# Kernel tuning notes

Measured on AMD Instinct MI355X. Metric: run time of the kernel, lower is better.

## Reference

```python
import jax, jax.numpy as jnp
import numpy as np

B, T, E = 4, 2048, 768
HN, HS = 12, 64          # head_num, head_size = E // HN
L = 6                    # n_layer
FF = 4 * E
O = 1                    # output_dim
EPS = 1e-5


def setup_inputs() -> dict:
    key = jax.random.key(0)
    ks = iter(jax.random.split(key, 40))
    r = lambda shape, s=0.02: jax.random.normal(next(ks), shape, jnp.float32) * s
    inp = {
        'idx': jax.random.normal(next(ks), (B, T, E), jnp.float32),
        'hidden': jnp.zeros((1, B, E), jnp.float32),
        # per-layer, per-head q/k/v linears
        'wq': r((L, HN, E, HS)), 'bq': jnp.zeros((L, HN, HS), jnp.float32),
        'wk': r((L, HN, E, HS)), 'bk': jnp.zeros((L, HN, HS), jnp.float32),
        'wv': r((L, HN, E, HS)), 'bv': jnp.zeros((L, HN, HS), jnp.float32),
        'wproj': r((L, E, E)), 'bproj': jnp.zeros((L, E), jnp.float32),
        'ln1_g': jnp.ones((L, E), jnp.float32), 'ln1_b': jnp.zeros((L, E), jnp.float32),
        'ln2_g': jnp.ones((L, E), jnp.float32), 'ln2_b': jnp.zeros((L, E), jnp.float32),
        'w1': r((L, E, FF)), 'b1': jnp.zeros((L, FF), jnp.float32),
        'w2': r((L, FF, E)), 'b2': jnp.zeros((L, E), jnp.float32),
        'lnf_g': jnp.ones((E,), jnp.float32), 'lnf_b': jnp.zeros((E,), jnp.float32),
        'fw1': r((E, FF)), 'fb1': jnp.zeros((FF,), jnp.float32),
        'fw2': r((FF, E)), 'fb2': jnp.zeros((E,), jnp.float32),
        'hw': r((E, O)), 'hb': jnp.zeros((O,), jnp.float32),
    }
    return inp


def _layernorm(x, g, b):
    m = jnp.mean(x, axis=-1, keepdims=True)
    v = jnp.var(x, axis=-1, keepdims=True)
    return (x - m) * jax.lax.rsqrt(v + EPS) * g + b


def _forward(idx, wq, bq, wk, bk, wv, bv, wproj, bproj,
             ln1_g, ln1_b, ln2_g, ln2_b, w1, b1, w2, b2,
             lnf_g, lnf_b, fw1, fb1, fw2, fb2, hw, hb):
    x = idx
    Bn, Tn, En = x.shape
    causal = jnp.tril(jnp.ones((Tn, Tn), bool))  # [T,T]
    scale = 1.0 / jnp.sqrt(jnp.asarray(En, x.dtype))  # NOTE: divides by sqrt(n_embed), as in source
    for l in range(wq.shape[0]):
        h = _layernorm(x, ln1_g[l], ln1_b[l])
        q = jnp.einsum('bte,hes->bhts', h, wq[l]) + bq[l][None, :, None, :]
        k = jnp.einsum('bte,hes->bhts', h, wk[l]) + bk[l][None, :, None, :]
        v = jnp.einsum('bte,hes->bhts', h, wv[l]) + bv[l][None, :, None, :]
        scores = jnp.einsum('bhts,bhus->bhtu', q, k) * scale
        scores = jnp.where(causal, scores, -jnp.inf)
        att = jax.nn.softmax(scores, axis=-1)
        o = jnp.einsum('bhtu,bhus->bhts', att, v)          # [B,HN,T,HS]
        o = o.transpose(0, 2, 1, 3).reshape(Bn, Tn, En)     # concat heads
        x = x + o @ wproj[l] + bproj[l]
        h = _layernorm(x, ln2_g[l], ln2_b[l])
        ff = jax.nn.gelu(h @ w1[l] + b1[l], approximate=False) @ w2[l] + b2[l]
        x = x + ff
    x = _layernorm(x, lnf_g, lnf_b)
    x = jax.nn.gelu(x @ fw1 + fb1, approximate=False) @ fw2 + fb2
    logits = x @ hw + hb            # [B,T,O]
    logits = logits[-1]             # [T,O]  (source: logits[-1,:,:])
    return jnp.squeeze(logits, axis=-1)  # [T]


def reference(idx, hidden, wq, bq, wk, bk, wv, bv, wproj, bproj,
              ln1_g, ln1_b, ln2_g, ln2_b, w1, b1, w2, b2,
              lnf_g, lnf_b, fw1, fb1, fw2, fb2, hw, hb):
    # hidden is accepted but unused by the original module.
    del hidden
    return _forward(idx, wq, bq, wk, bk, wv, bv, wproj, bproj,
                    ln1_g, ln1_b, ln2_g, ln2_b, w1, b1, w2, b2,
                    lnf_g, lnf_b, fw1, fb1, fw2, fb2, hw, hb)
```

## Files before the change

### kernel.cpp

```cpp
#include <hip/hip_runtime.h>
#include <math.h>

#define TT 2048
#define EE 768
#define HNN 12
#define HSS 64
#define NLAYER 6
#define FFD 3072
#define QKVN 2304

constexpr float LN_EPS = 1e-5f;
constexpr float ATT_SCALE = 0.03608439182435161f;
constexpr float ATT_SCALE_L2E = 0.03608439182435161f * 1.4426950408889634f;

typedef __attribute__((ext_vector_type(8))) short bf16x8;
typedef __attribute__((ext_vector_type(4))) float f32x4;

__device__ __forceinline__ ushort f2bf(float f) {
    union { float f; uint u; } c; c.f = f;
    const uint u = c.u;
    return (ushort)((u + 0x7fffu + ((u >> 16) & 1u)) >> 16);
}

__device__ __forceinline__ void gload16(const void* g, void* l) {
    __builtin_amdgcn_global_load_lds((const __attribute__((address_space(1))) void*)g,
                                     (__attribute__((address_space(3))) void*)l, 16, 0, 0);
}

__global__ __launch_bounds__(256) void copy4_kernel(float4* __restrict__ dst,
                                                    const float4* __restrict__ src, int n4) {
    int i = blockIdx.x * 256 + threadIdx.x;
    if (i < n4) dst[i] = src[i];
}

__global__ __launch_bounds__(256) void ln_kernel(const float* __restrict__ in,
                                                 const float* __restrict__ g,
                                                 const float* __restrict__ b,
                                                 ushort* __restrict__ out) {
    __shared__ float red[8];
    const int t = blockIdx.x;
    const int tid = threadIdx.x;
    const float* row = in + (size_t)t * EE;
    float v0 = row[tid], v1 = row[tid + 256], v2 = row[tid + 512];
    float s = v0 + v1 + v2;
#pragma unroll
    for (int m = 1; m < 64; m <<= 1) s += __shfl_xor(s, m, 64);
    if ((tid & 63) == 0) red[tid >> 6] = s;
    __syncthreads();
    const float mean = (red[0] + red[1] + red[2] + red[3]) * (1.0f / EE);
    const float d0 = v0 - mean, d1 = v1 - mean, d2 = v2 - mean;
    float qq = d0 * d0 + d1 * d1 + d2 * d2;
#pragma unroll
    for (int m = 1; m < 64; m <<= 1) qq += __shfl_xor(qq, m, 64);
    __syncthreads();
    if ((tid & 63) == 0) red[tid >> 6] = qq;
    __syncthreads();
    const float var = (red[0] + red[1] + red[2] + red[3]) * (1.0f / EE);
    const float rstd = rsqrtf(var + LN_EPS);
    ushort* orow = out + (size_t)t * EE;
    orow[tid]       = f2bf(d0 * rstd * g[tid]       + b[tid]);
    orow[tid + 256] = f2bf(d1 * rstd * g[tid + 256] + b[tid + 256]);
    orow[tid + 512] = f2bf(d2 * rstd * g[tid + 512] + b[tid + 512]);
}

__device__ __forceinline__ void transpose64(const float* __restrict__ src, int sld,
                                            ushort* __restrict__ dst, int dld,
                                            int k0, int n0, int tid) {
    __shared__ float t[64][68];
#pragma unroll
    for (int p = 0; p < 4; p++) {
        const int kr = p * 16 + (tid >> 4);
        *(float4*)&t[kr][(tid & 15) * 4] =
            *(const float4*)&src[(size_t)(k0 + kr) * sld + n0 + (tid & 15) * 4];
    }
    __syncthreads();
#pragma unroll
    for (int q = 0; q < 2; q++) {
        const int nl = q * 32 + (tid >> 3);
        const int kc = (tid & 7) * 8;
        ushort v[8];
#pragma unroll
        for (int j = 0; j < 8; j++) v[j] = f2bf(t[kc + j][nl]);
        uint4 o;
        o.x = (uint)v[0] | ((uint)v[1] << 16);
        o.y = (uint)v[2] | ((uint)v[3] << 16);
        o.z = (uint)v[4] | ((uint)v[5] << 16);
        o.w = (uint)v[6] | ((uint)v[7] << 16);
        *(uint4*)&dst[(size_t)(n0 + nl) * dld + k0 + kc] = o;
    }
}

__global__ __launch_bounds__(256) void pack_t_kernel(const float* __restrict__ src, int sld,
                                                     ushort* __restrict__ dst, int dld) {
    transpose64(src, sld, dst, dld, blockIdx.x * 64, blockIdx.y * 64, threadIdx.x);
}

__global__ __launch_bounds__(256) void pack_qkv_kernel(const float* __restrict__ wq,
                                                       const float* __restrict__ wk,
                                                       const float* __restrict__ wv,
                                                       ushort* __restrict__ dst) {
    const int z = blockIdx.z;
    const int which = z / HNN, hd = z % HNN;
    const float* src = (which == 0 ? wq : which == 1 ? wk : wv) + (size_t)hd * EE * HSS;
    ushort* d = dst + (size_t)(which * EE + hd * HSS) * EE;
    transpose64(src, HSS, d, EE, blockIdx.x * 64, 0, threadIdx.x);
}

__global__ __launch_bounds__(256) void vtrans_kernel(const ushort* __restrict__ qkv,
                                                     ushort* __restrict__ vT) {
    const int t = blockIdx.x * 256 + threadIdx.x;
    const int d = t & 63;
    const int rest = t >> 6;
    const int tb = rest & 255;
    const int hd = rest >> 8;
    const ushort* src = qkv + 1536 + hd * 64 + d;
    ushort v[8];
#pragma unroll
    for (int j = 0; j < 8; j++) v[j] = src[(size_t)(tb * 8 + j) * QKVN];
    uint4 o;
    o.x = (uint)v[0] | ((uint)v[1] << 16);
    o.y = (uint)v[2] | ((uint)v[3] << 16);
    o.z = (uint)v[4] | ((uint)v[5] << 16);
    o.w = (uint)v[6] | ((uint)v[7] << 16);
    *(uint4*)&vT[((size_t)hd * 64 + d) * TT + tb * 8] = o;
}

template <int EPI>
__global__ __launch_bounds__(256) void gemm_bf16(const ushort* __restrict__ A,
                                                 const ushort* __restrict__ Bt,
                                                 const float* __restrict__ b0,
                                                 const float* __restrict__ b1,
                                                 const float* __restrict__ b2,
                                                 float* __restrict__ outF,
                                                 ushort* __restrict__ outB,
                                                 int N, int K,
                                                 int nby, int KS, int Kslice) {
    __shared__ ushort Al[2][128 * 32];
    __shared__ ushort Bl[2][128 * 32];
    const int tid = threadIdx.x;
    const int wave = tid >> 6, lane = tid & 63;
    const int wm = wave >> 1, wn = wave & 1;
    const int l15 = lane & 15, q4 = lane >> 4;

    const int nwg = gridDim.x;
    const int wgid = ((int)blockIdx.x & 7) * (nwg >> 3) + ((int)blockIdx.x >> 3);
    const int mb = wgid % nby;
    const int t2 = wgid / nby;
    const int ks = t2 % KS;
    const int nb = t2 / KS;
    const int m0 = mb * 128, n0 = nb * 128;
    const int kbase = ks * Kslice;

    const int srow = lane >> 2;
    const int scb = (lane & 3) ^ ((lane >> 3) & 3);
    const ushort* Ag0 = A + (size_t)(m0 + wave * 16 + srow) * K + kbase + scb * 8;
    const ushort* Ag1 = Ag0 + (size_t)64 * K;
    const ushort* Bg0 = Bt + (size_t)(n0 + wave * 16 + srow) * K + kbase + scb * 8;
    const ushort* Bg1 = Bg0 + (size_t)64 * K;

    auto stage = [&](int buf, int kk) {
        const int off = kk * 32;
        gload16(Ag0 + off, &Al[buf][(wave * 16) * 32]);
        gload16(Ag1 + off, &Al[buf][(64 + wave * 16) * 32]);
        gload16(Bg0 + off, &Bl[buf][(wave * 16) * 32]);
        gload16(Bg1 + off, &Bl[buf][(64 + wave * 16) * 32]);
    };

    f32x4 acc[4][4];
#pragma unroll
    for (int i = 0; i < 4; i++)
#pragma unroll
        for (int j = 0; j < 4; j++) acc[i][j] = (f32x4){0.f, 0.f, 0.f, 0.f};

    stage(0, 0);
    __syncthreads();

    const int niter = Kslice >> 5;
    const int cq = (q4 ^ ((l15 >> 1) & 3)) * 8;

    for (int i = 0; i < niter; i++) {
        const int buf = i & 1;
        if (i + 1 < niter) stage(buf ^ 1, i + 1);
        bf16x8 af[4], bfr[4];
#pragma unroll
        for (int ii = 0; ii < 4; ii++)
            af[ii] = *(const bf16x8*)&Al[buf][(wm * 64 + ii * 16 + l15) * 32 + cq];
#pragma unroll
        for (int j = 0; j < 4; j++)
            bfr[j] = *(const bf16x8*)&Bl[buf][(wn * 64 + j * 16 + l15) * 32 + cq];
#pragma unroll
        for (int ii = 0; ii < 4; ii++)
#pragma unroll
            for (int j = 0; j < 4; j++)
                acc[ii][j] = __builtin_amdgcn_mfma_f32_16x16x32_bf16(af[ii], bfr[j], acc[ii][j], 0, 0, 0);
        __syncthreads();
    }

#pragma unroll
    for (int i = 0; i < 4; i++) {
        const int row = m0 + wm * 64 + i * 16 + q4 * 4;
#pragma unroll
        for (int j = 0; j < 4; j++) {
            const int col = n0 + wn * 64 + j * 16 + l15;
            float bias;
            if constexpr (EPI == 0)
                bias = (col < 768) ? b0[col] : (col < 1536 ? b1[col - 768] : b2[col - 1536]);
            else
                bias = (EPI == 1 && ks != 0) ? 0.f : b0[col];
#pragma unroll
            for (int r = 0; r < 4; r++) {
                const float v = acc[i][j][r] + bias;
                const size_t idx = (size_t)(row + r) * N + col;
                if constexpr (EPI == 0) {
                    outB[idx] = f2bf(v);
                } else if constexpr (EPI == 1) {
                    atomicAdd(&outF[idx], v);
                } else if constexpr (EPI == 2) {
                    outB[idx] = f2bf(0.5f * v * (1.0f + erff(v * 0.70710678118654752f)));
                } else {
                    outF[idx] = v;
                }
            }
        }
    }
}

__global__ __launch_bounds__(256, 2) void attn_mfma(const ushort* __restrict__ qkv,
                                                    const ushort* __restrict__ vT,
                                                    ushort* __restrict__ o_bf) {
    __shared__ __align__(16) uint Ps[4][16 * 36];

    const int tid = threadIdx.x;
    const int wave = tid >> 6, lane = tid & 63;
    const int l15 = lane & 15, q4 = lane >> 4;

    const int x = (int)blockIdx.x & 7, r = (int)blockIdx.x >> 3;
    const int rho = wave * 48 + r;
    int head, qi;
    if (rho < 128) { head = x;           qi = 127 - rho; }
    else           { head = 8 + (x >> 1); qi = 2 * (191 - rho) + (x & 1); }
    const int nkt = (qi >> 2) + 1;
    const int qrow_g = qi * 16 + l15;

    const ushort* qp = qkv + (size_t)qrow_g * QKVN + head * 64;
    const bf16x8 qa0 = *(const bf16x8*)&qp[q4 * 8];
    const bf16x8 qa1 = *(const bf16x8*)&qp[32 + q4 * 8];

    const ushort* kbase = qkv + 768 + head * 64 + (size_t)l15 * QKVN + q4 * 8;
    const ushort* vbase = vT + ((size_t)head * 64 + l15) * TT + q4 * 8;

    float m_i = -1e30f, l_i = 0.f;
    f32x4 oacc[4];
#pragma unroll
    for (int n = 0; n < 4; n++) oacc[n] = (f32x4){0.f, 0.f, 0.f, 0.f};

    bf16x8 kA[8], kB[8], vC[8];
#pragma unroll
    for (int n = 0; n < 4; n++)
#pragma unroll
        for (int kb = 0; kb < 2; kb++)
            kA[n * 2 + kb] = *(const bf16x8*)(kbase + (size_t)(n * 16) * QKVN + kb * 32);

    uint* psrow = &Ps[wave][l15 * 36];

    auto body = [&](bf16x8* kc, bf16x8* kn, int kt) {
        const ushort* vp = vbase + kt * 64;
#pragma unroll
        for (int n = 0; n < 4; n++)
#pragma unroll
            for (int kb = 0; kb < 2; kb++)
                vC[n * 2 + kb] = *(const bf16x8*)(vp + (size_t)(n * 16) * TT + kb * 32);
        if (kt + 1 < nkt) {
            const ushort* kp = kbase + (size_t)(kt + 1) * 64 * QKVN;
#pragma unroll
            for (int n = 0; n < 4; n++)
#pragma unroll
                for (int kb = 0; kb < 2; kb++)
                    kn[n * 2 + kb] = *(const bf16x8*)(kp + (size_t)(n * 16) * QKVN + kb * 32);
        }
        f32x4 s[4];
#pragma unroll
        for (int n = 0; n < 4; n++) {
            f32x4 a = (f32x4){0.f, 0.f, 0.f, 0.f};
            a = __builtin_amdgcn_mfma_f32_16x16x32_bf16(kc[n * 2], qa0, a, 0, 0, 0);
            a = __builtin_amdgcn_mfma_f32_16x16x32_bf16(kc[n * 2 + 1], qa1, a, 0, 0, 0);
            s[n] = a;
        }
        float pe[16];
        const bool diag = (kt == nkt - 1);
#pragma unroll
        for (int n = 0; n < 4; n++) {
            const int k0 = kt * 64 + n * 16 + q4 * 4;
#pragma unroll
            for (int rr = 0; rr < 4; rr++) {
                float xv = s[n][rr] * ATT_SCALE_L2E;
                if (diag && (k0 + rr) > qrow_g) xv = -1e30f;
                pe[n * 4 + rr] = xv;
            }
        }
        float t8[8];
#pragma unroll
        for (int i = 0; i < 8; i++) t8[i] = fmaxf(pe[i], pe[i + 8]);
        float mx = fmaxf(fmaxf(fmaxf(t8[0], t8[4]), fmaxf(t8[1], t8[5])),
                         fmaxf(fmaxf(t8[2], t8[6]), fmaxf(t8[3], t8[7])));
        mx = fmaxf(mx, __shfl_xor(mx, 16, 64));
        mx = fmaxf(mx, __shfl_xor(mx, 32, 64));
        const float nm = fmaxf(m_i, mx);
        const float al = exp2f(m_i - nm);
#pragma unroll
        for (int i = 0; i < 16; i++) pe[i] = exp2f(pe[i] - nm);
        float s8[8];
#pragma unroll
        for (int i = 0; i < 8; i++) s8[i] = pe[i] + pe[i + 8];
        float rs = ((s8[0] + s8[4]) + (s8[1] + s8[5])) + ((s8[2] + s8[6]) + (s8[3] + s8[7]));
        rs += __shfl_xor(rs, 16, 64);
        rs += __shfl_xor(rs, 32, 64);
        l_i = l_i * al + rs;
        m_i = nm;
        float alr[4];
#pragma unroll
        for (int rr = 0; rr < 4; rr++) alr[rr] = __shfl(al, q4 * 4 + rr, 64);
#pragma unroll
        for (int n = 0; n < 4; n++) {
            oacc[n][0] *= alr[0];
            oacc[n][1] *= alr[1];
            oacc[n][2] *= alr[2];
            oacc[n][3] *= alr[3];
        }
#pragma unroll
        for (int n = 0; n < 4; n++) {
            uint2 d2;
            d2.x = (uint)f2bf(pe[n * 4 + 0]) | ((uint)f2bf(pe[n * 4 + 1]) << 16);
            d2.y = (uint)f2bf(pe[n * 4 + 2]) | ((uint)f2bf(pe[n * 4 + 3]) << 16);
            *(uint2*)&psrow[(8 * n + 2 * q4 + 4 * l15) & 31] = d2;
        }
        const bf16x8 pa0 = *(const bf16x8*)&psrow[(4 * q4 + 4 * l15) & 31];
        const bf16x8 pa1 = *(const bf16x8*)&psrow[(16 + 4 * q4 + 4 * l15) & 31];
#pragma unroll
        for (int n = 0; n < 4; n++) {
            oacc[n] = __builtin_amdgcn_mfma_f32_16x16x32_bf16(pa0, vC[n * 2], oacc[n], 0, 0, 0);
            oacc[n] = __builtin_amdgcn_mfma_f32_16x16x32_bf16(pa1, vC[n * 2 + 1], oacc[n], 0, 0, 0);
        }
    };

    int kt = 0;
    for (;;) {
        body(kA, kB, kt);
        if (++kt >= nkt) break;
        body(kB, kA, kt);
        if (++kt >= nkt) break;
    }

    float lrec[4];
#pragma unroll
    for (int rr = 0; rr < 4; rr++) lrec[rr] = 1.0f / __shfl(l_i, q4 * 4 + rr, 64);
#pragma unroll
    for (int n = 0; n < 4; n++)
#pragma unroll
        for (int rr = 0; rr < 4; rr++)
            o_bf[(size_t)(qi * 16 + q4 * 4 + rr) * EE + head * 64 + n * 16 + l15] =
                f2bf(oacc[n][rr] * lrec[rr]);
}

__global__ __launch_bounds__(256) void head_kernel(const float* __restrict__ x,
                                                   const float* __restrict__ hw,
                                                   const float* __restrict__ hb,
                                                   float* __restrict__ out) {
    __shared__ float red[8];
    const int t = blockIdx.x, tid = threadIdx.x;
    const float* row = x + (size_t)t * EE;
    float s = row[tid] * hw[tid] + row[tid + 256] * hw[tid + 256] + row[tid + 512] * hw[tid + 512];
#pragma unroll
    for (int m = 1; m < 64; m <<= 1) s += __shfl_xor(s, m, 64);
    if ((tid & 63) == 0) red[tid >> 6] = s;
    __syncthreads();
    if (tid == 0) out[t] = red[0] + red[1] + red[2] + red[3] + hb[0];
}

extern "C" void kernel_launch(void* const* d_in, const int* in_sizes, int n_in,
                              void* d_out, int out_size, void* d_ws, size_t ws_size,
                              hipStream_t stream) {
    const float* idx   = (const float*)d_in[0];
    const float* wq    = (const float*)d_in[2];
    const float* bq    = (const float*)d_in[3];
    const float* wk    = (const float*)d_in[4];
    const float* bk    = (const float*)d_in[5];
    const float* wv    = (const float*)d_in[6];
    const float* bv    = (const float*)d_in[7];
    const float* wproj = (const float*)d_in[8];
    const float* bproj = (const float*)d_in[9];
    const float* ln1g  = (const float*)d_in[10];
    const float* ln1b  = (const float*)d_in[11];
    const float* ln2g  = (const float*)d_in[12];
    const float* ln2b  = (const float*)d_in[13];
    const float* w1    = (const float*)d_in[14];
    const float* b1    = (const float*)d_in[15];
    const float* w2    = (const float*)d_in[16];
    const float* b2    = (const float*)d_in[17];
    const float* lnfg  = (const float*)d_in[18];
    const float* lnfb  = (const float*)d_in[19];
    const float* fw1   = (const float*)d_in[20];
    const float* fb1   = (const float*)d_in[21];
    const float* fw2   = (const float*)d_in[22];
    const float* fb2   = (const float*)d_in[23];
    const float* hw    = (const float*)d_in[24];
    const float* hb    = (const float*)d_in[25];
    float* out = (float*)d_out;

    char* p = (char*)d_ws;
    auto alloc = [&](size_t bytes) { void* r = (void*)p; p += (bytes + 255) & ~(size_t)255; return r; };
    float*  x     = (float*)alloc((size_t)TT * EE * 4);
    ushort* h_bf  = (ushort*)alloc((size_t)TT * EE * 2);
    ushort* qkvb  = (ushort*)alloc((size_t)TT * QKVN * 2);
    ushort* o_bf  = (ushort*)alloc((size_t)TT * EE * 2);
    ushort* ffb   = (ushort*)alloc((size_t)TT * FFD * 2);
    ushort* Wqkv  = (ushort*)alloc((size_t)QKVN * EE * 2);
    ushort* Wproj = (ushort*)alloc((size_t)EE * EE * 2);
    ushort* W1t   = (ushort*)alloc((size_t)FFD * EE * 2);
    ushort* W2t   = (ushort*)alloc((size_t)EE * FFD * 2);
    ushort* vTb   = (ushort*)alloc((size_t)HNN * HSS * TT * 2);

    copy4_kernel<<<dim3((TT * EE / 4 + 255) / 256), dim3(256), 0, stream>>>(
        (float4*)x, (const float4*)(idx + (size_t)3 * TT * EE), TT * EE / 4);

    for (int l = 0; l < NLAYER; l++) {
        const size_t lw = (size_t)l;
        pack_qkv_kernel<<<dim3(12, 1, 36), dim3(256), 0, stream>>>(
            wq + lw * HNN * EE * HSS, wk + lw * HNN * EE * HSS, wv + lw * HNN * EE * HSS, Wqkv);
        pack_t_kernel<<<dim3(12, 12), dim3(256), 0, stream>>>(wproj + lw * EE * EE, EE, Wproj, EE);
        pack_t_kernel<<<dim3(12, 48), dim3(256), 0, stream>>>(w1 + lw * EE * FFD, FFD, W1t, EE);
        pack_t_kernel<<<dim3(48, 12), dim3(256), 0, stream>>>(w2 + lw * FFD * EE, EE, W2t, FFD);

        ln_kernel<<<dim3(TT), dim3(256), 0, stream>>>(x, ln1g + lw * EE, ln1b + lw * EE, h_bf);
        gemm_bf16<0><<<dim3(288), dim3(256), 0, stream>>>(
            h_bf, Wqkv, bq + lw * EE, bk + lw * EE, bv + lw * EE, nullptr, qkvb,
            QKVN, EE, 16, 1, EE);
        vtrans_kernel<<<dim3(768), dim3(256), 0, stream>>>(qkvb, vTb);
        attn_mfma<<<dim3(384), dim3(256), 0, stream>>>(qkvb, vTb, o_bf);
        gemm_bf16<1><<<dim3(384), dim3(256), 0, stream>>>(
            o_bf, Wproj, bproj + lw * EE, nullptr, nullptr, x, nullptr,
            EE, EE, 16, 4, 192);
        ln_kernel<<<dim3(TT), dim3(256), 0, stream>>>(x, ln2g + lw * EE, ln2b + lw * EE, h_bf);
        gemm_bf16<2><<<dim3(384), dim3(256), 0, stream>>>(
            h_bf, W1t, b1 + lw * FFD, nullptr, nullptr, nullptr, ffb,
            FFD, EE, 16, 1, EE);
        gemm_bf16<1><<<dim3(384), dim3(256), 0, stream>>>(
            ffb, W2t, b2 + lw * EE, nullptr, nullptr, x, nullptr,
            EE, FFD, 16, 4, 768);
    }

    ln_kernel<<<dim3(TT), dim3(256), 0, stream>>>(x, lnfg, lnfb, h_bf);
    pack_t_kernel<<<dim3(12, 48), dim3(256), 0, stream>>>(fw1, FFD, W1t, EE);
    pack_t_kernel<<<dim3(48, 12), dim3(256), 0, stream>>>(fw2, EE, W2t, FFD);
    gemm_bf16<2><<<dim3(384), dim3(256), 0, stream>>>(
        h_bf, W1t, fb1, nullptr, nullptr, nullptr, ffb, FFD, EE, 16, 1, EE);
    gemm_bf16<3><<<dim3(96), dim3(256), 0, stream>>>(
        ffb, W2t, fb2, nullptr, nullptr, x, nullptr, EE, FFD, 16, 1, FFD);
    head_kernel<<<dim3(TT), dim3(256), 0, stream>>>(x, hw, hb, out);
}
```

Before: 1.620 ms.

## Split long causal attention rows across KV chunks with combine kernel

Attention work is now split into fixed 12-tile KV chunks. Query tiles beyond the first 48 are divided into 2 or 3 partial chunks whose unnormalized outputs and m/l statistics go to a scratch buffer, aliased on the FFN buffer. A new combine kernel merges the partials in flash-decoding style. This evens out per-wave work across the causal triangle and raises occupancy hints, at the cost of an extra launch and extra fp32 traffic through global memory.

```diff
diff --git a/kernel.cpp b/kernel.cpp
--- a/kernel.cpp
+++ b/kernel.cpp
@@ -225,21 +225,27 @@
     }
 }
 
-__global__ __launch_bounds__(256, 2) void attn_mfma(const ushort* __restrict__ qkv,
+__global__ __launch_bounds__(256, 4) void attn_mfma(const ushort* __restrict__ qkv,
                                                     const ushort* __restrict__ vT,
-                                                    ushort* __restrict__ o_bf) {
+                                                    ushort* __restrict__ o_bf,
+                                                    float* __restrict__ pbuf) {
     __shared__ __align__(16) uint Ps[4][16 * 36];
 
     const int tid = threadIdx.x;
     const int wave = tid >> 6, lane = tid & 63;
     const int l15 = lane & 15, q4 = lane >> 4;
 
-    const int x = (int)blockIdx.x & 7, r = (int)blockIdx.x >> 3;
-    const int rho = wave * 48 + r;
-    int head, qi;
-    if (rho < 128) { head = x;           qi = 127 - rho; }
-    else           { head = 8 + (x >> 1); qi = 2 * (191 - rho) + (x & 1); }
+    const int chunk = (int)blockIdx.x * 4 + wave;
+    const int head = chunk / 240;
+    const int t = chunk - head * 240;
+    int qi, c;
+    if (t < 48) { qi = t; c = 0; }
+    else if (t < 144) { const int u = t - 48; qi = 48 + (u >> 1); c = u & 1; }
+    else { const int u = t - 144; const int q3 = u / 3; qi = 96 + q3; c = u - q3 * 3; }
     const int nkt = (qi >> 2) + 1;
+    const int kt_begin = c * 12;
+    const int kt_end = min(kt_begin + 12, nkt);
+    const bool direct = (qi < 48);
     const int qrow_g = qi * 16 + l15;
 
     const ushort* qp = qkv + (size_t)qrow_g * QKVN + head * 64;
@@ -255,11 +261,14 @@
     for (int n = 0; n < 4; n++) oacc[n] = (f32x4){0.f, 0.f, 0.f, 0.f};
 
     bf16x8 kA[8], kB[8], vC[8];
-#pragma unroll
-    for (int n = 0; n < 4; n++)
-#pragma unroll
-        for (int kb = 0; kb < 2; kb++)
-            kA[n * 2 + kb] = *(const bf16x8*)(kbase + (size_t)(n * 16) * QKVN + kb * 32);
+    {
+        const ushort* kp = kbase + (size_t)kt_begin * 64 * QKVN;
+#pragma unroll
+        for (int n = 0; n < 4; n++)
+#pragma unroll
+            for (int kb = 0; kb < 2; kb++)
+                kA[n * 2 + kb] = *(const bf16x8*)(kp + (size_t)(n * 16) * QKVN + kb * 32);
+    }
 
     uint* psrow = &Ps[wave][l15 * 36];
 
@@ -270,7 +279,7 @@
 #pragma unroll
             for (int kb = 0; kb < 2; kb++)
                 vC[n * 2 + kb] = *(const bf16x8*)(vp + (size_t)(n * 16) * TT + kb * 32);
-        if (kt + 1 < nkt) {
+        if (kt + 1 < kt_end) {
             const ushort* kp = kbase + (size_t)(kt + 1) * 64 * QKVN;
 #pragma unroll
             for (int n = 0; n < 4; n++)
@@ -343,23 +352,64 @@
         }
     };
 
-    int kt = 0;
+    int kt = kt_begin;
     for (;;) {
         body(kA, kB, kt);
-        if (++kt >= nkt) break;
+        if (++kt >= kt_end) break;
         body(kB, kA, kt);
-        if (++kt >= nkt) break;
-    }
-
-    float lrec[4];
-#pragma unroll
-    for (int rr = 0; rr < 4; rr++) lrec[rr] = 1.0f / __shfl(l_i, q4 * 4 + rr, 64);
-#pragma unroll
-    for (int n = 0; n < 4; n++)
-#pragma unroll
-        for (int rr = 0; rr < 4; rr++)
-            o_bf[(size_t)(qi * 16 + q4 * 4 + rr) * EE + head * 64 + n * 16 + l15] =
-                f2bf(oacc[n][rr] * lrec[rr]);
+        if (++kt >= kt_end) break;
+    }
+
+    if (direct) {
+        float lrec[4];
+#pragma unroll
+        for (int rr = 0; rr < 4; rr++) lrec[rr] = 1.0f / __shfl(l_i, q4 * 4 + rr, 64);
+#pragma unroll
+        for (int n = 0; n < 4; n++)
+#pragma unroll
+            for (int rr = 0; rr < 4; rr++)
+                o_bf[(size_t)(qi * 16 + q4 * 4 + rr) * EE + head * 64 + n * 16 + l15] =
+                    f2bf(oacc[n][rr] * lrec[rr]);
+    } else {
+        float* pb = pbuf + (size_t)((head * 80 + (qi - 48)) * 3 + c) * 1056;
+#pragma unroll
+        for (int n = 0; n < 4; n++)
+#pragma unroll
+            for (int rr = 0; rr < 4; rr++)
+                pb[(q4 * 4 + rr) * 64 + n * 16 + l15] = oacc[n][rr];
+        if (q4 == 0) {
+            pb[1024 + l15] = m_i;
+            pb[1040 + l15] = l_i;
+        }
+    }
+}
+
+__global__ __launch_bounds__(256) void attn_combine(const float* __restrict__ pbuf,
+                                                    ushort* __restrict__ o_bf) {
+    const int wave = threadIdx.x >> 6, lane = threadIdx.x & 63;
+    const int task = (int)blockIdx.x * 4 + wave;
+    const int head = task / 80;
+    const int u = task - head * 80;
+    const int qi = 48 + u;
+    const int nc = (qi < 96) ? 2 : 3;
+    const float* pb = pbuf + (size_t)((head * 80 + u) * 3) * 1056;
+
+    for (int r = 0; r < 16; r++) {
+        float m0 = pb[1024 + r];
+        float m1 = pb[1056 + 1024 + r];
+        float m2 = (nc == 3) ? pb[2112 + 1024 + r] : -1e30f;
+        const float M = fmaxf(fmaxf(m0, m1), m2);
+        const float w0 = exp2f(m0 - M);
+        const float w1 = exp2f(m1 - M);
+        const float w2 = (nc == 3) ? exp2f(m2 - M) : 0.f;
+        float L = w0 * pb[1040 + r] + w1 * pb[1056 + 1040 + r];
+        float v = w0 * pb[r * 64 + lane] + w1 * pb[1056 + r * 64 + lane];
+        if (nc == 3) {
+            L += w2 * pb[2112 + 1040 + r];
+            v += w2 * pb[2112 + r * 64 + lane];
+        }
+        o_bf[(size_t)(qi * 16 + r) * EE + head * 64 + lane] = f2bf(v / L);
+    }
 }
 
 __global__ __launch_bounds__(256) void head_kernel(const float* __restrict__ x,
@@ -419,6 +469,7 @@
     ushort* W1t   = (ushort*)alloc((size_t)FFD * EE * 2);
     ushort* W2t   = (ushort*)alloc((size_t)EE * FFD * 2);
     ushort* vTb   = (ushort*)alloc((size_t)HNN * HSS * TT * 2);
+    float* pbuf = (float*)ffb;
 
     copy4_kernel<<<dim3((TT * EE / 4 + 255) / 256), dim3(256), 0, stream>>>(
         (float4*)x, (const float4*)(idx + (size_t)3 * TT * EE), TT * EE / 4);
@@ -436,7 +487,8 @@
             h_bf, Wqkv, bq + lw * EE, bk + lw * EE, bv + lw * EE, nullptr, qkvb,
             QKVN, EE, 16, 1, EE);
         vtrans_kernel<<<dim3(768), dim3(256), 0, stream>>>(qkvb, vTb);
-        attn_mfma<<<dim3(384), dim3(256), 0, stream>>>(qkvb, vTb, o_bf);
+        attn_mfma<<<dim3(720), dim3(256), 0, stream>>>(qkvb, vTb, o_bf, pbuf);
+        attn_combine<<<dim3(240), dim3(256), 0, stream>>>(pbuf, o_bf);
         gemm_bf16<1><<<dim3(384), dim3(256), 0, stream>>>(
             o_bf, Wproj, bproj + lw * EE, nullptr, nullptr, x, nullptr,
             EE, EE, 16, 4, 192);
```

New measurement: 1.851 ms. +14.3%, slower.

## Split attention KV range across waves with shared-memory softmax merge

Applied to the files above, without the earlier changes.

Each block now handles one 16-row query tile, and its four waves each process a contiguous quarter of the causal KV tiles (split-K flash attention). Partial outputs, maxima and sums are combined through shared memory with a log-sum-exp merge, and the grid grows from 384 to 1536 blocks. The launch bound is raised to 4 blocks per SM. This is meant to cut the per-wave serial KV loop length and improve load balance and latency hiding. In exchange it adds LDS traffic, a block barrier, and idle waves on short rows where there are fewer than four KV tiles.

```diff
diff --git a/kernel.cpp b/kernel.cpp
--- a/kernel.cpp
+++ b/kernel.cpp
@@ -225,21 +225,26 @@
     }
 }
 
-__global__ __launch_bounds__(256, 2) void attn_mfma(const ushort* __restrict__ qkv,
+__global__ __launch_bounds__(256, 4) void attn_mfma(const ushort* __restrict__ qkv,
                                                     const ushort* __restrict__ vT,
                                                     ushort* __restrict__ o_bf) {
-    __shared__ __align__(16) uint Ps[4][16 * 36];
+    __shared__ __align__(16) uint  Ps[4][16 * 36];
+    __shared__ __align__(16) float Po[4][16 * 64];
+    __shared__ float Pm[4][16];
+    __shared__ float Pl[4][16];
 
     const int tid = threadIdx.x;
     const int wave = tid >> 6, lane = tid & 63;
     const int l15 = lane & 15, q4 = lane >> 4;
 
     const int x = (int)blockIdx.x & 7, r = (int)blockIdx.x >> 3;
-    const int rho = wave * 48 + r;
     int head, qi;
-    if (rho < 128) { head = x;           qi = 127 - rho; }
-    else           { head = 8 + (x >> 1); qi = 2 * (191 - rho) + (x & 1); }
+    if (r < 128) { head = x;            qi = 127 - r; }
+    else         { head = 8 + (x >> 1); qi = 2 * (191 - r) + (x & 1); }
     const int nkt = (qi >> 2) + 1;
+    const int per = (nkt + 3) >> 2;
+    const int kt0 = wave * per;
+    const int kt1 = min(kt0 + per, nkt);
     const int qrow_g = qi * 16 + l15;
 
     const ushort* qp = qkv + (size_t)qrow_g * QKVN + head * 64;
@@ -254,112 +259,140 @@
 #pragma unroll
     for (int n = 0; n < 4; n++) oacc[n] = (f32x4){0.f, 0.f, 0.f, 0.f};
 
-    bf16x8 kA[8], kB[8], vC[8];
+    uint* psrow = &Ps[wave][l15 * 36];
+
+    if (kt0 < kt1) {
+        bf16x8 kA[8], kB[8], vC[8];
+        {
+            const ushort* kp = kbase + (size_t)kt0 * 64 * QKVN;
+#pragma unroll
+            for (int n = 0; n < 4; n++)
+#pragma unroll
+                for (int kb = 0; kb < 2; kb++)
+                    kA[n * 2 + kb] = *(const bf16x8*)(kp + (size_t)(n * 16) * QKVN + kb * 32);
+        }
+
+        auto body = [&](bf16x8* kc, bf16x8* kn, int kt) {
+            const ushort* vp = vbase + kt * 64;
+#pragma unroll
+            for (int n = 0; n < 4; n++)
+#pragma unroll
+                for (int kb = 0; kb < 2; kb++)
+                    vC[n * 2 + kb] = *(const bf16x8*)(vp + (size_t)(n * 16) * TT + kb * 32);
+            if (kt + 1 < kt1) {
+                const ushort* kp = kbase + (size_t)(kt + 1) * 64 * QKVN;
+#pragma unroll
+                for (int n = 0; n < 4; n++)
+#pragma unroll
+                    for (int kb = 0; kb < 2; kb++)
+                        kn[n * 2 + kb] = *(const bf16x8*)(kp + (size_t)(n * 16) * QKVN + kb * 32);
+            }
+            f32x4 s[4];
+#pragma unroll
+            for (int n = 0; n < 4; n++) {
+                f32x4 a = (f32x4){0.f, 0.f, 0.f, 0.f};
+                a = __builtin_amdgcn_mfma_f32_16x16x32_bf16(kc[n * 2], qa0, a, 0, 0, 0);
+                a = __builtin_amdgcn_mfma_f32_16x16x32_bf16(kc[n * 2 + 1], qa1, a, 0, 0, 0);
+                s[n] = a;
+            }
+            float pe[16];
+            const bool diag = (kt == nkt - 1);
+#pragma unroll
+            for (int n = 0; n < 4; n++) {
+                const int k0 = kt * 64 + n * 16 + q4 * 4;
+#pragma unroll
+                for (int rr = 0; rr < 4; rr++) {
+                    float xv = s[n][rr] * ATT_SCALE_L2E;
+                    if (diag && (k0 + rr) > qrow_g) xv = -1e30f;
+                    pe[n * 4 + rr] = xv;
+                }
+            }
+            float t8[8];
+#pragma unroll
+            for (int i = 0; i < 8; i++) t8[i] = fmaxf(pe[i], pe[i + 8]);
+            float mx = fmaxf(fmaxf(fmaxf(t8[0], t8[4]), fmaxf(t8[1], t8[5])),
+                             fmaxf(fmaxf(t8[2], t8[6]), fmaxf(t8[3], t8[7])));
+            mx = fmaxf(mx, __shfl_xor(mx, 16, 64));
+            mx = fmaxf(mx, __shfl_xor(mx, 32, 64));
+            const float nm = fmaxf(m_i, mx);
+            const float al = exp2f(m_i - nm);
+#pragma unroll
+            for (int i = 0; i < 16; i++) pe[i] = exp2f(pe[i] - nm);
+            float s8[8];
+#pragma unroll
+            for (int i = 0; i < 8; i++) s8[i] = pe[i] + pe[i + 8];
+            float rs = ((s8[0] + s8[4]) + (s8[1] + s8[5])) + ((s8[2] + s8[6]) + (s8[3] + s8[7]));
+            rs += __shfl_xor(rs, 16, 64);
+            rs += __shfl_xor(rs, 32, 64);
+            l_i = l_i * al + rs;
+            m_i = nm;
+            float alr[4];
+#pragma unroll
+            for (int rr = 0; rr < 4; rr++) alr[rr] = __shfl(al, q4 * 4 + rr, 64);
+#pragma unroll
+            for (int n = 0; n < 4; n++) {
+                oacc[n][0] *= alr[0];
+                oacc[n][1] *= alr[1];
+                oacc[n][2] *= alr[2];
+                oacc[n][3] *= alr[3];
+            }
+#pragma unroll
+            for (int n = 0; n < 4; n++) {
+                uint2 d2;
+                d2.x = (uint)f2bf(pe[n * 4 + 0]) | ((uint)f2bf(pe[n * 4 + 1]) << 16);
+                d2.y = (uint)f2bf(pe[n * 4 + 2]) | ((uint)f2bf(pe[n * 4 + 3]) << 16);
+                *(uint2*)&psrow[(8 * n + 2 * q4 + 4 * l15) & 31] = d2;
+            }
+            const bf16x8 pa0 = *(const bf16x8*)&psrow[(4 * q4 + 4 * l15) & 31];
+            const bf16x8 pa1 = *(const bf16x8*)&psrow[(16 + 4 * q4 + 4 * l15) & 31];
+#pragma unroll
+            for (int n = 0; n < 4; n++) {
+                oacc[n] = __builtin_amdgcn_mfma_f32_16x16x32_bf16(pa0, vC[n * 2], oacc[n], 0, 0, 0);
+                oacc[n] = __builtin_amdgcn_mfma_f32_16x16x32_bf16(pa1, vC[n * 2 + 1], oacc[n], 0, 0, 0);
+            }
+        };
+
+        int kt = kt0;
+        for (;;) {
+            body(kA, kB, kt);
+            if (++kt >= kt1) break;
+            body(kB, kA, kt);
+            if (++kt >= kt1) break;
+        }
+    }
+
 #pragma unroll
     for (int n = 0; n < 4; n++)
 #pragma unroll
-        for (int kb = 0; kb < 2; kb++)
-            kA[n * 2 + kb] = *(const bf16x8*)(kbase + (size_t)(n * 16) * QKVN + kb * 32);
-
-    uint* psrow = &Ps[wave][l15 * 36];
-
-    auto body = [&](bf16x8* kc, bf16x8* kn, int kt) {
-        const ushort* vp = vbase + kt * 64;
-#pragma unroll
-        for (int n = 0; n < 4; n++)
-#pragma unroll
-            for (int kb = 0; kb < 2; kb++)
-                vC[n * 2 + kb] = *(const bf16x8*)(vp + (size_t)(n * 16) * TT + kb * 32);
-        if (kt + 1 < nkt) {
-            const ushort* kp = kbase + (size_t)(kt + 1) * 64 * QKVN;
-#pragma unroll
-            for (int n = 0; n < 4; n++)
-#pragma unroll
-                for (int kb = 0; kb < 2; kb++)
-                    kn[n * 2 + kb] = *(const bf16x8*)(kp + (size_t)(n * 16) * QKVN + kb * 32);
-        }
-        f32x4 s[4];
-#pragma unroll
-        for (int n = 0; n < 4; n++) {
-            f32x4 a = (f32x4){0.f, 0.f, 0.f, 0.f};
-            a = __builtin_amdgcn_mfma_f32_16x16x32_bf16(kc[n * 2], qa0, a, 0, 0, 0);
-            a = __builtin_amdgcn_mfma_f32_16x16x32_bf16(kc[n * 2 + 1], qa1, a, 0, 0, 0);
-            s[n] = a;
-        }
-        float pe[16];
-        const bool diag = (kt == nkt - 1);
-#pragma unroll
-        for (int n = 0; n < 4; n++) {
-            const int k0 = kt * 64 + n * 16 + q4 * 4;
-#pragma unroll
-            for (int rr = 0; rr < 4; rr++) {
-                float xv = s[n][rr] * ATT_SCALE_L2E;
-                if (diag && (k0 + rr) > qrow_g) xv = -1e30f;
-                pe[n * 4 + rr] = xv;
-            }
-        }
-        float t8[8];
-#pragma unroll
-        for (int i = 0; i < 8; i++) t8[i] = fmaxf(pe[i], pe[i + 8]);
-        float mx = fmaxf(fmaxf(fmaxf(t8[0], t8[4]), fmaxf(t8[1], t8[5])),
-                         fmaxf(fmaxf(t8[2], t8[6]), fmaxf(t8[3], t8[7])));
-        mx = fmaxf(mx, __shfl_xor(mx, 16, 64));
-        mx = fmaxf(mx, __shfl_xor(mx, 32, 64));
-        const float nm = fmaxf(m_i, mx);
-        const float al = exp2f(m_i - nm);
-#pragma unroll
-        for (int i = 0; i < 16; i++) pe[i] = exp2f(pe[i] - nm);
-        float s8[8];
-#pragma unroll
-        for (int i = 0; i < 8; i++) s8[i] = pe[i] + pe[i + 8];
-        float rs = ((s8[0] + s8[4]) + (s8[1] + s8[5])) + ((s8[2] + s8[6]) + (s8[3] + s8[7]));
-        rs += __shfl_xor(rs, 16, 64);
-        rs += __shfl_xor(rs, 32, 64);
-        l_i = l_i * al + rs;
-        m_i = nm;
-        float alr[4];
-#pragma unroll
-        for (int rr = 0; rr < 4; rr++) alr[rr] = __shfl(al, q4 * 4 + rr, 64);
-#pragma unroll
-        for (int n = 0; n < 4; n++) {
-            oacc[n][0] *= alr[0];
-            oacc[n][1] *= alr[1];
-            oacc[n][2] *= alr[2];
-            oacc[n][3] *= alr[3];
-        }
-#pragma unroll
-        for (int n = 0; n < 4; n++) {
-            uint2 d2;
-            d2.x = (uint)f2bf(pe[n * 4 + 0]) | ((uint)f2bf(pe[n * 4 + 1]) << 16);
-            d2.y = (uint)f2bf(pe[n * 4 + 2]) | ((uint)f2bf(pe[n * 4 + 3]) << 16);
-            *(uint2*)&psrow[(8 * n + 2 * q4 + 4 * l15) & 31] = d2;
-        }
-        const bf16x8 pa0 = *(const bf16x8*)&psrow[(4 * q4 + 4 * l15) & 31];
-        const bf16x8 pa1 = *(const bf16x8*)&psrow[(16 + 4 * q4 + 4 * l15) & 31];
-#pragma unroll
-        for (int n = 0; n < 4; n++) {
-            oacc[n] = __builtin_amdgcn_mfma_f32_16x16x32_bf16(pa0, vC[n * 2], oacc[n], 0, 0, 0);
-            oacc[n] = __builtin_amdgcn_mfma_f32_16x16x32_bf16(pa1, vC[n * 2 + 1], oacc[n], 0, 0, 0);
-        }
-    };
-
-    int kt = 0;
-    for (;;) {
-        body(kA, kB, kt);
-        if (++kt >= nkt) break;
-        body(kB, kA, kt);
-        if (++kt >= nkt) break;
-    }
-
-    float lrec[4];
-#pragma unroll
-    for (int rr = 0; rr < 4; rr++) lrec[rr] = 1.0f / __shfl(l_i, q4 * 4 + rr, 64);
-#pragma unroll
-    for (int n = 0; n < 4; n++)
-#pragma unroll
         for (int rr = 0; rr < 4; rr++)
-            o_bf[(size_t)(qi * 16 + q4 * 4 + rr) * EE + head * 64 + n * 16 + l15] =
-                f2bf(oacc[n][rr] * lrec[rr]);
+            Po[wave][(q4 * 4 + rr) * 64 + n * 16 + l15] = oacc[n][rr];
+    if (q4 == 0) {
+        Pm[wave][l15] = m_i;
+        Pl[wave][l15] = l_i;
+    }
+    __syncthreads();
+
+    const int row = tid >> 4;
+    const int c4 = (tid & 15) * 4;
+    const float m0 = Pm[0][row], m1 = Pm[1][row], m2 = Pm[2][row], m3 = Pm[3][row];
+    const float M = fmaxf(fmaxf(m0, m1), fmaxf(m2, m3));
+    const float w0 = exp2f(m0 - M), w1 = exp2f(m1 - M), w2 = exp2f(m2 - M), w3 = exp2f(m3 - M);
+    const float L = w0 * Pl[0][row] + w1 * Pl[1][row] + w2 * Pl[2][row] + w3 * Pl[3][row];
+    const f32x4 o0 = *(const f32x4*)&Po[0][row * 64 + c4];
+    const f32x4 o1 = *(const f32x4*)&Po[1][row * 64 + c4];
+    const f32x4 o2 = *(const f32x4*)&Po[2][row * 64 + c4];
+    const f32x4 o3 = *(const f32x4*)&Po[3][row * 64 + c4];
+    const float rl = 1.0f / L;
+    uint2 ow;
+    {
+        const float v0 = (w0 * o0[0] + w1 * o1[0] + w2 * o2[0] + w3 * o3[0]) * rl;
+        const float v1 = (w0 * o0[1] + w1 * o1[1] + w2 * o2[1] + w3 * o3[1]) * rl;
+        const float v2 = (w0 * o0[2] + w1 * o1[2] + w2 * o2[2] + w3 * o3[2]) * rl;
+        const float v3 = (w0 * o0[3] + w1 * o1[3] + w2 * o2[3] + w3 * o3[3]) * rl;
+        ow.x = (uint)f2bf(v0) | ((uint)f2bf(v1) << 16);
+        ow.y = (uint)f2bf(v2) | ((uint)f2bf(v3) << 16);
+    }
+    *(uint2*)&o_bf[(size_t)(qi * 16 + row) * EE + head * 64 + c4] = ow;
 }
 
 __global__ __launch_bounds__(256) void head_kernel(const float* __restrict__ x,
@@ -436,7 +469,7 @@
             h_bf, Wqkv, bq + lw * EE, bk + lw * EE, bv + lw * EE, nullptr, qkvb,
             QKVN, EE, 16, 1, EE);
         vtrans_kernel<<<dim3(768), dim3(256), 0, stream>>>(qkvb, vTb);
-        attn_mfma<<<dim3(384), dim3(256), 0, stream>>>(qkvb, vTb, o_bf);
+        attn_mfma<<<dim3(1536), dim3(256), 0, stream>>>(qkvb, vTb, o_bf);
         gemm_bf16<1><<<dim3(384), dim3(256), 0, stream>>>(
             o_bf, Wproj, bproj + lw * EE, nullptr, nullptr, x, nullptr,
             EE, EE, 16, 4, 192);
```

Measured after the change: 1.681 ms. +3.8%, slower.
